# Kernel optimization log

Measured on AMD Instinct MI355X. Metric: run time of the kernel, lower is better.

## Reference

```python
import jax, jax.numpy as jnp
import numpy as np

S = 8      # max segment id present in masks
D = 768    # hidden size (hardcoded in the torch module)
N_VIS = 100  # leading vision tokens in vision_trace_feat


def _segment_mean(feat, mask, n_seg):
    """Per-(batch, seg_id) mean of feat tokens where mask == seg_id.
    feat: [B, L, D], mask: [B, L] ints in 0..n_seg. Returns means [B, n_seg, D], counts [B, n_seg].
    Equivalent to the torch loop over seg_id + split + per-chunk mean(dim=0)."""
    onehot = (mask[:, :, None] == jnp.arange(1, n_seg + 1)[None, None, :]).astype(feat.dtype)  # [B,L,S]
    sums = jnp.einsum('bls,bld->bsd', onehot, feat)   # [B,S,D]
    counts = onehot.sum(axis=1)                        # [B,S]
    means = sums / jnp.maximum(counts, 1.0)[:, :, None]
    return means, counts


def setup_inputs() -> dict:
    key = jax.random.key(0)
    k1, k2, k3, k4, k5, k6 = jax.random.split(key, 6)
    B = 64
    vision_trace_feat = jax.random.normal(k1, (B, N_VIS + 412, D), dtype=jnp.float32)
    vision_trace_mask = jnp.sort(jax.random.randint(k2, (B, 412), 0, S + 1), axis=-1).astype(jnp.int32)
    caption_feat = jax.random.normal(k3, (B, 512, D), dtype=jnp.float32)
    caption_mask = jnp.sort(jax.random.randint(k4, (B, 513), 0, S + 1), axis=-1).astype(jnp.int32)
    vt_merge_w = jax.random.normal(k5, (2 * D, D), dtype=jnp.float32) * 0.02
    vt_merge_b = jax.random.normal(k6, (D,), dtype=jnp.float32) * 0.02
    return {
        'vision_trace_feat': vision_trace_feat,
        'vision_trace_mask': vision_trace_mask,
        'caption_feat': caption_feat,
        'caption_mask': caption_mask,
        'vt_merge_w': vt_merge_w,
        'vt_merge_b': vt_merge_b,
    }


def reference(vision_trace_feat, vision_trace_mask, caption_feat, caption_mask, vt_merge_w, vt_merge_b):
    # --- CaptionAggregator (meanpool) ---
    cm = caption_mask[:, 1:]                                   # drop CLS position
    c_means, c_counts = _segment_mean(caption_feat, cm, S)      # [B,S,D], [B,S]
    c_present = (c_counts > 0).astype(c_means.dtype)
    caption_out = c_means * c_present[:, :, None]               # dense form: empty segments zeroed

    # --- VisionTraceAggregator (meanpool) ---
    vision_feat = vision_trace_feat[:, :N_VIS].mean(axis=1)     # [B,D]
    trace_feat = vision_trace_feat[:, N_VIS:]                   # [B,Lt,D]
    t_means, t_counts = _segment_mean(trace_feat, vision_trace_mask, S)
    t_present = (t_counts > 0).astype(t_means.dtype)
    vt = jnp.concatenate(
        [t_means, jnp.broadcast_to(vision_feat[:, None, :], t_means.shape)], axis=-1)  # [B,S,2D]
    vt_out = (vt @ vt_merge_w + vt_merge_b) * t_present[:, :, None]
    return (caption_out, vt_out)
```

## Files before the change

### kernel.cpp

```cpp
#include <hip/hip_runtime.h>
#include <hip/hip_bf16.h>

#define SEGS   8
#define DIM    768
#define NVIS   100
#define BATCH  64
#define LTOK   512
#define NCHK   8
#define TPC    64

#define OFF_PCAP  0
#define OFF_PTRC  (OFF_PCAP + BATCH*NCHK*SEGS*DIM)
#define OFF_PVIS  (OFF_PTRC + BATCH*NCHK*SEGS*DIM)
#define OFF_PCCNT (OFF_PVIS + BATCH*2*DIM)
#define OFF_PTCNT (OFF_PCCNT + BATCH*NCHK*SEGS)
#define OFF_TMEAN (OFF_PTCNT + BATCH*NCHK*SEGS)
#define OFF_TCNT  (OFF_TMEAN + BATCH*9*DIM)


__global__ __launch_bounds__(384) void reduce_kernel(
    const float* __restrict__ vt_feat,
    const int* __restrict__ vt_mask,
    const float* __restrict__ cap_feat,
    const int* __restrict__ cap_mask,
    float* __restrict__ ws)
{
    const int bid  = blockIdx.x;
    const int type = bid >> 9;
    const int b    = (bid >> 3) & 63;
    const int ck   = bid & 7;
    const int tid  = threadIdx.x;
    const int team = tid / 192;
    const int t    = tid % 192;
    const int c0   = t * 4;

    __shared__ __align__(16) int msk[TPC];
    __shared__ int scnt[SEGS + 1];
    __shared__ __align__(16) float4 red[SEGS][192];
    __shared__ __align__(16) float4 redv[192];

    if (tid < SEGS + 1) scnt[tid] = 0;
    if (tid < TPC) {
        const int l = ck * TPC + tid;
        int m;
        if (type == 0) m = cap_mask[b * 513 + 1 + l];
        else           m = (l >= NVIS) ? vt_mask[b * 412 + (l - NVIS)] : 0;
        msk[tid] = m;
    }
    __syncthreads();
    if (tid < TPC) { const int m = msk[tid]; if (m > 0) atomicAdd(&scnt[m], 1); }

    float acc[SEGS][4];
#pragma unroll
    for (int s = 0; s < SEGS; ++s) { acc[s][0]=0.f; acc[s][1]=0.f; acc[s][2]=0.f; acc[s][3]=0.f; }
    float vacc[4] = {0.f, 0.f, 0.f, 0.f};
    float tmp[4]  = {0.f, 0.f, 0.f, 0.f};
    int cur = 0;

    const float* __restrict__ feat = (type == 0) ? cap_feat : vt_feat;
    const int tok0 = ck * TPC + team * 32;
    const size_t base = (size_t)b * LTOK * DIM + (size_t)c0;

    for (int j = 0; j < 32; j += 4) {
        const float* p = feat + base + (size_t)(tok0 + j) * DIM;
        float4 v[4];
#pragma unroll
        for (int u = 0; u < 4; ++u)
            v[u] = *reinterpret_cast<const float4*>(p + (size_t)u * DIM);
        const int4 m4 = *reinterpret_cast<const int4*>(&msk[team * 32 + j]);
        const int mm[4] = {m4.x, m4.y, m4.z, m4.w};
#pragma unroll
        for (int u = 0; u < 4; ++u) {
            const int l = tok0 + j + u;
            if (type == 1 && l < NVIS) {
                vacc[0] += v[u].x; vacc[1] += v[u].y; vacc[2] += v[u].z; vacc[3] += v[u].w;
            } else {
                const int m = __builtin_amdgcn_readfirstlane(mm[u]);
                if (m != cur) {
#pragma unroll
                    for (int s = 0; s < SEGS; ++s)
                        if (cur == s + 1) {
                            acc[s][0] += tmp[0]; acc[s][1] += tmp[1];
                            acc[s][2] += tmp[2]; acc[s][3] += tmp[3];
                        }
                    tmp[0] = 0.f; tmp[1] = 0.f; tmp[2] = 0.f; tmp[3] = 0.f;
                    cur = m;
                }
                tmp[0] += v[u].x; tmp[1] += v[u].y; tmp[2] += v[u].z; tmp[3] += v[u].w;
            }
        }
    }
#pragma unroll
    for (int s = 0; s < SEGS; ++s)
        if (cur == s + 1) {
            acc[s][0] += tmp[0]; acc[s][1] += tmp[1];
            acc[s][2] += tmp[2]; acc[s][3] += tmp[3];
        }

    if (team == 1) {
#pragma unroll
        for (int s = 0; s < SEGS; ++s)
            red[s][t] = make_float4(acc[s][0], acc[s][1], acc[s][2], acc[s][3]);
        redv[t] = make_float4(vacc[0], vacc[1], vacc[2], vacc[3]);
    }
    __syncthreads();

    if (team == 0) {
        float* __restrict__ pbase = ws + (type == 0 ? OFF_PCAP : OFF_PTRC)
                                  + ((size_t)(b * NCHK + ck) * SEGS) * DIM + c0;
#pragma unroll
        for (int s = 0; s < SEGS; ++s) {
            const float4 r1 = red[s][t];
            *reinterpret_cast<float4*>(pbase + s * DIM) =
                make_float4(acc[s][0] + r1.x, acc[s][1] + r1.y,
                            acc[s][2] + r1.z, acc[s][3] + r1.w);
        }
        if (t < SEGS) {
            int* __restrict__ cbase = (int*)(ws + (type == 0 ? OFF_PCCNT : OFF_PTCNT))
                                    + (b * NCHK + ck) * SEGS;
            cbase[t] = scnt[t + 1];
        }
        if (type == 1 && ck < 2) {
            const float4 r1 = redv[t];
            *reinterpret_cast<float4*>(ws + OFF_PVIS + (size_t)(b * 2 + ck) * DIM + c0) =
                make_float4(vacc[0] + r1.x, vacc[1] + r1.y,
                            vacc[2] + r1.z, vacc[3] + r1.w);
        }
    }
}

__global__ __launch_bounds__(256) void combine1_kernel(
    const float* __restrict__ ws_c, float* __restrict__ ws,
    float* __restrict__ out)
{
    const int i = blockIdx.x * 256 + threadIdx.x;
    const int N1 = BATCH * SEGS * DIM / 4;
    if (i < N1) {
        const int b  = i / 1536;
        const int r  = i % 1536;
        const int s  = r / 192;
        const int d4 = (r % 192) * 4;
        float4 sum = make_float4(0.f, 0.f, 0.f, 0.f); int c = 0;
#pragma unroll
        for (int ck = 0; ck < NCHK; ++ck) {
            const float4 v = *reinterpret_cast<const float4*>(
                ws_c + OFF_PCAP + ((size_t)((b * NCHK + ck) * SEGS + s)) * DIM + d4);
            sum.x += v.x; sum.y += v.y; sum.z += v.z; sum.w += v.w;
            c += ((const int*)(ws_c + OFF_PCCNT))[(b * NCHK + ck) * SEGS + s];
        }
        float4 o = make_float4(0.f, 0.f, 0.f, 0.f);
        if (c > 0) {
            const float fc = (float)c;
            o = make_float4(sum.x / fc, sum.y / fc, sum.z / fc, sum.w / fc);
        }
        reinterpret_cast<float4*>(out)[i] = o;
    } else if (i < 2 * N1) {
        const int j  = i - N1;
        const int b  = j / 1536;
        const int r  = j % 1536;
        const int s  = r / 192;
        const int d4 = (r % 192) * 4;
        float4 sum = make_float4(0.f, 0.f, 0.f, 0.f); int c = 0;
#pragma unroll
        for (int ck = 0; ck < NCHK; ++ck) {
            const float4 v = *reinterpret_cast<const float4*>(
                ws_c + OFF_PTRC + ((size_t)((b * NCHK + ck) * SEGS + s)) * DIM + d4);
            sum.x += v.x; sum.y += v.y; sum.z += v.z; sum.w += v.w;
            c += ((const int*)(ws_c + OFF_PTCNT))[(b * NCHK + ck) * SEGS + s];
        }
        float4 m = make_float4(0.f, 0.f, 0.f, 0.f);
        if (c > 0) {
            const float fc = (float)c;
            m = make_float4(sum.x / fc, sum.y / fc, sum.z / fc, sum.w / fc);
        }
        *reinterpret_cast<float4*>(ws + OFF_TMEAN + ((size_t)(b * 9 + s)) * DIM + d4) = m;
        if (d4 == 0) ((int*)(ws + OFF_TCNT))[b * SEGS + s] = c;
    } else {
        const int j  = i - 2 * N1;
        const int b  = j / 192;
        const int d4 = (j % 192) * 4;
        const float4 v0 = *reinterpret_cast<const float4*>(
            ws_c + OFF_PVIS + (size_t)(b * 2 + 0) * DIM + d4);
        const float4 v1 = *reinterpret_cast<const float4*>(
            ws_c + OFF_PVIS + (size_t)(b * 2 + 1) * DIM + d4);
        const float sc = 1.0f / (float)NVIS;
        *reinterpret_cast<float4*>(ws + OFF_TMEAN + ((size_t)(b * 9 + 8)) * DIM + d4) =
            make_float4((v0.x + v1.x) * sc, (v0.y + v1.y) * sc,
                        (v0.z + v1.z) * sc, (v0.w + v1.w) * sc);
    }
}

__global__ __launch_bounds__(192) void gemm2_kernel(
    const float* __restrict__ W,
    const float* __restrict__ bias,
    const float* __restrict__ ws_c,
    float* __restrict__ out)
{
    const int b   = blockIdx.x >> 3;
    const int nc  = blockIdx.x & 7;
    const int n0  = nc * 96;
    const int tid = threadIdx.x;
    const int cg  = tid % 24;
    const int kq  = tid / 24;
    const int d0  = n0 + cg * 4;

    __shared__ __align__(16) float tm[9 * 8 * 100];
    __shared__ __align__(16) float red[192 * 9 * 4];

    for (int idx = tid; idx < 9 * DIM / 4; idx += 192) {
        const int r   = idx / 192;
        const int rem = idx % 192;
        const int kq_ = rem / 24;
        const int kk4 = rem % 24;
        const float4 v = reinterpret_cast<const float4*>(
            ws_c + OFF_TMEAN + (size_t)b * 9 * DIM)[idx];
        *reinterpret_cast<float4*>(&tm[(r * 8 + kq_) * 100 + kk4 * 4]) = v;
    }
    __syncthreads();

    float acc[9][4];
#pragma unroll
    for (int r = 0; r < 9; ++r) { acc[r][0]=0.f; acc[r][1]=0.f; acc[r][2]=0.f; acc[r][3]=0.f; }

    const float* __restrict__ Wt = W + (size_t)(kq * 96) * DIM + d0;
    const float* __restrict__ Wb = W + (size_t)(DIM + kq * 96) * DIM + d0;

    for (int kk = 0; kk < 96; kk += 4) {
        float4 wt[4], wb[4];
#pragma unroll
        for (int u = 0; u < 4; ++u) {
            wt[u] = *reinterpret_cast<const float4*>(Wt + (size_t)(kk + u) * DIM);
            wb[u] = *reinterpret_cast<const float4*>(Wb + (size_t)(kk + u) * DIM);
        }
        float a[9][4];
#pragma unroll
        for (int r = 0; r < 9; ++r) {
            const float4 t = *reinterpret_cast<const float4*>(&tm[(r * 8 + kq) * 100 + kk]);
            a[r][0] = t.x; a[r][1] = t.y; a[r][2] = t.z; a[r][3] = t.w;
        }
#pragma unroll
        for (int u = 0; u < 4; ++u) {
            const float t4[4] = {wt[u].x, wt[u].y, wt[u].z, wt[u].w};
            const float b4[4] = {wb[u].x, wb[u].y, wb[u].z, wb[u].w};
#pragma unroll
            for (int r = 0; r < SEGS; ++r) {
#pragma unroll
                for (int j = 0; j < 4; ++j) acc[r][j] += a[r][u] * t4[j];
            }
#pragma unroll
            for (int j = 0; j < 4; ++j) acc[8][j] += a[8][u] * b4[j];
        }
    }

#pragma unroll
    for (int r = 0; r < 9; ++r)
        *reinterpret_cast<float4*>(&red[(tid * 9 + r) * 4]) =
            make_float4(acc[r][0], acc[r][1], acc[r][2], acc[r][3]);
    __syncthreads();

    {
        const int cg2 = tid >> 3;
        const int s   = tid & 7;
        float4 sumS = make_float4(0.f, 0.f, 0.f, 0.f);
        float4 sumV = make_float4(0.f, 0.f, 0.f, 0.f);
#pragma unroll
        for (int q = 0; q < 8; ++q) {
            const int base = (q * 24 + cg2) * 9;
            const float4 vS = *reinterpret_cast<const float4*>(&red[(base + s) * 4]);
            const float4 vV = *reinterpret_cast<const float4*>(&red[(base + 8) * 4]);
            sumS.x += vS.x; sumS.y += vS.y; sumS.z += vS.z; sumS.w += vS.w;
            sumV.x += vV.x; sumV.y += vV.y; sumV.z += vV.z; sumV.w += vV.w;
        }
        const int dd = n0 + cg2 * 4;
        const int c  = ((const int*)(ws_c + OFF_TCNT))[b * SEGS + s];
        float4 o = make_float4(0.f, 0.f, 0.f, 0.f);
        if (c > 0) {
            const float4 bb = *reinterpret_cast<const float4*>(bias + dd);
            o = make_float4(sumS.x + sumV.x + bb.x, sumS.y + sumV.y + bb.y,
                            sumS.z + sumV.z + bb.z, sumS.w + sumV.w + bb.w);
        }
        *reinterpret_cast<float4*>(out + (size_t)BATCH * SEGS * DIM
                                   + ((size_t)(b * SEGS + s)) * DIM + dd) = o;
    }
}

extern "C" void kernel_launch(void* const* d_in, const int* in_sizes, int n_in,
                              void* d_out, int out_size, void* d_ws, size_t ws_size,
                              hipStream_t stream) {
    const float* vt_feat  = (const float*)d_in[0];
    const int*   vt_mask  = (const int*)d_in[1];
    const float* cap_feat = (const float*)d_in[2];
    const int*   cap_mask = (const int*)d_in[3];
    const float* W        = (const float*)d_in[4];
    const float* bias     = (const float*)d_in[5];
    float* out = (float*)d_out;
    float* ws = (float*)d_ws;

    reduce_kernel  <<<1024, 384, 0, stream>>>(vt_feat, vt_mask, cap_feat, cap_mask, ws);
    combine1_kernel<<<816, 256, 0, stream>>>(ws, ws, out);
    gemm2_kernel   <<<512, 192, 0, stream>>>(W, bias, ws, out);
}
```

Baseline: 260.6 us.

## Fuse segment reduction and combine into one kernel splitting by column blocks

Replaces the token-chunked reduce kernel plus combine kernel with a single kernel where each block owns a batch and a 256-column slice over all 512 tokens. Eight wavefront teams reduce through shared memory and write the final means directly, which removes the partial-sum workspace round trip and one kernel launch. Each team also skips its leading run of zero-mask tokens, since those contribute to no segment. The cost is fewer blocks (384 instead of 1024) and more shared memory per block, which may lower the parallelism available for streaming the feature data.

New measurement: 251.4 us. 1.04x faster.

```diff
diff --git a/kernel.cpp b/kernel.cpp
--- a/kernel.cpp
+++ b/kernel.cpp
@@ -6,49 +6,57 @@
 #define NVIS   100
 #define BATCH  64
 #define LTOK   512
-#define NCHK   8
-#define TPC    64
-
-#define OFF_PCAP  0
-#define OFF_PTRC  (OFF_PCAP + BATCH*NCHK*SEGS*DIM)
-#define OFF_PVIS  (OFF_PTRC + BATCH*NCHK*SEGS*DIM)
-#define OFF_PCCNT (OFF_PVIS + BATCH*2*DIM)
-#define OFF_PTCNT (OFF_PCCNT + BATCH*NCHK*SEGS)
-#define OFF_TMEAN (OFF_PTCNT + BATCH*NCHK*SEGS)
+
+#define OFF_TMEAN 0
 #define OFF_TCNT  (OFF_TMEAN + BATCH*9*DIM)
 
 
-__global__ __launch_bounds__(384) void reduce_kernel(
+__global__ __launch_bounds__(512) void reduce_merge_kernel(
     const float* __restrict__ vt_feat,
     const int* __restrict__ vt_mask,
     const float* __restrict__ cap_feat,
     const int* __restrict__ cap_mask,
-    float* __restrict__ ws)
+    float* __restrict__ ws,
+    float* __restrict__ out)
 {
     const int bid  = blockIdx.x;
-    const int type = bid >> 9;
-    const int b    = (bid >> 3) & 63;
-    const int ck   = bid & 7;
+    const int type = bid / 192;
+    const int rr   = bid % 192;
+    const int b    = rr / 3;
+    const int cb   = rr % 3;
     const int tid  = threadIdx.x;
-    const int team = tid / 192;
-    const int t    = tid % 192;
-    const int c0   = t * 4;
-
-    __shared__ __align__(16) int msk[TPC];
+    const int team = tid >> 6;
+    const int t    = tid & 63;
+    const int c0   = cb * 256 + t * 4;
+
+    __shared__ __align__(16) int msk[LTOK];
     __shared__ int scnt[SEGS + 1];
-    __shared__ __align__(16) float4 red[SEGS][192];
-    __shared__ __align__(16) float4 redv[192];
+    __shared__ __align__(16) float4 red[7][SEGS][64];
+    __shared__ __align__(16) float4 redv[7][64];
 
     if (tid < SEGS + 1) scnt[tid] = 0;
-    if (tid < TPC) {
-        const int l = ck * TPC + tid;
-        int m;
-        if (type == 0) m = cap_mask[b * 513 + 1 + l];
-        else           m = (l >= NVIS) ? vt_mask[b * 412 + (l - NVIS)] : 0;
-        msk[tid] = m;
-    }
-    __syncthreads();
-    if (tid < TPC) { const int m = msk[tid]; if (m > 0) atomicAdd(&scnt[m], 1); }
+    int m0;
+    {
+        const int l = tid;
+        if (type == 0) m0 = cap_mask[b * 513 + 1 + l];
+        else           m0 = (l >= NVIS) ? vt_mask[b * 412 + (l - NVIS)] : 0;
+        msk[l] = m0;
+    }
+    __syncthreads();
+    if (m0 > 0) atomicAdd(&scnt[m0], 1);
+
+    const int tok0 = team * 64;
+    int j0 = 0;
+    if (type == 0) {
+        while (j0 < 64 && msk[tok0 + j0] == 0) ++j0;
+    } else {
+        while (j0 < 64) {
+            const int l = tok0 + j0;
+            if (l < NVIS || msk[l] > 0) break;
+            ++j0;
+        }
+    }
+    j0 &= ~3;
 
     float acc[SEGS][4];
 #pragma unroll
@@ -58,16 +66,15 @@
     int cur = 0;
 
     const float* __restrict__ feat = (type == 0) ? cap_feat : vt_feat;
-    const int tok0 = ck * TPC + team * 32;
     const size_t base = (size_t)b * LTOK * DIM + (size_t)c0;
 
-    for (int j = 0; j < 32; j += 4) {
+    for (int j = j0; j < 64; j += 4) {
         const float* p = feat + base + (size_t)(tok0 + j) * DIM;
         float4 v[4];
 #pragma unroll
         for (int u = 0; u < 4; ++u)
             v[u] = *reinterpret_cast<const float4*>(p + (size_t)u * DIM);
-        const int4 m4 = *reinterpret_cast<const int4*>(&msk[team * 32 + j]);
+        const int4 m4 = *reinterpret_cast<const int4*>(&msk[tok0 + j]);
         const int mm[4] = {m4.x, m4.y, m4.z, m4.w};
 #pragma unroll
         for (int u = 0; u < 4; ++u) {
@@ -97,96 +104,60 @@
             acc[s][2] += tmp[2]; acc[s][3] += tmp[3];
         }
 
-    if (team == 1) {
+    if (team > 0) {
 #pragma unroll
         for (int s = 0; s < SEGS; ++s)
-            red[s][t] = make_float4(acc[s][0], acc[s][1], acc[s][2], acc[s][3]);
-        redv[t] = make_float4(vacc[0], vacc[1], vacc[2], vacc[3]);
+            red[team - 1][s][t] = make_float4(acc[s][0], acc[s][1], acc[s][2], acc[s][3]);
+        redv[team - 1][t] = make_float4(vacc[0], vacc[1], vacc[2], vacc[3]);
     }
     __syncthreads();
 
     if (team == 0) {
-        float* __restrict__ pbase = ws + (type == 0 ? OFF_PCAP : OFF_PTRC)
-                                  + ((size_t)(b * NCHK + ck) * SEGS) * DIM + c0;
 #pragma unroll
         for (int s = 0; s < SEGS; ++s) {
-            const float4 r1 = red[s][t];
-            *reinterpret_cast<float4*>(pbase + s * DIM) =
-                make_float4(acc[s][0] + r1.x, acc[s][1] + r1.y,
-                            acc[s][2] + r1.z, acc[s][3] + r1.w);
-        }
-        if (t < SEGS) {
-            int* __restrict__ cbase = (int*)(ws + (type == 0 ? OFF_PCCNT : OFF_PTCNT))
-                                    + (b * NCHK + ck) * SEGS;
-            cbase[t] = scnt[t + 1];
-        }
-        if (type == 1 && ck < 2) {
-            const float4 r1 = redv[t];
-            *reinterpret_cast<float4*>(ws + OFF_PVIS + (size_t)(b * 2 + ck) * DIM + c0) =
-                make_float4(vacc[0] + r1.x, vacc[1] + r1.y,
-                            vacc[2] + r1.z, vacc[3] + r1.w);
-        }
-    }
-}
-
-__global__ __launch_bounds__(256) void combine1_kernel(
-    const float* __restrict__ ws_c, float* __restrict__ ws,
-    float* __restrict__ out)
-{
-    const int i = blockIdx.x * 256 + threadIdx.x;
-    const int N1 = BATCH * SEGS * DIM / 4;
-    if (i < N1) {
-        const int b  = i / 1536;
-        const int r  = i % 1536;
-        const int s  = r / 192;
-        const int d4 = (r % 192) * 4;
-        float4 sum = make_float4(0.f, 0.f, 0.f, 0.f); int c = 0;
-#pragma unroll
-        for (int ck = 0; ck < NCHK; ++ck) {
-            const float4 v = *reinterpret_cast<const float4*>(
-                ws_c + OFF_PCAP + ((size_t)((b * NCHK + ck) * SEGS + s)) * DIM + d4);
-            sum.x += v.x; sum.y += v.y; sum.z += v.z; sum.w += v.w;
-            c += ((const int*)(ws_c + OFF_PCCNT))[(b * NCHK + ck) * SEGS + s];
-        }
-        float4 o = make_float4(0.f, 0.f, 0.f, 0.f);
-        if (c > 0) {
-            const float fc = (float)c;
-            o = make_float4(sum.x / fc, sum.y / fc, sum.z / fc, sum.w / fc);
-        }
-        reinterpret_cast<float4*>(out)[i] = o;
-    } else if (i < 2 * N1) {
-        const int j  = i - N1;
-        const int b  = j / 1536;
-        const int r  = j % 1536;
-        const int s  = r / 192;
-        const int d4 = (r % 192) * 4;
-        float4 sum = make_float4(0.f, 0.f, 0.f, 0.f); int c = 0;
-#pragma unroll
-        for (int ck = 0; ck < NCHK; ++ck) {
-            const float4 v = *reinterpret_cast<const float4*>(
-                ws_c + OFF_PTRC + ((size_t)((b * NCHK + ck) * SEGS + s)) * DIM + d4);
-            sum.x += v.x; sum.y += v.y; sum.z += v.z; sum.w += v.w;
-            c += ((const int*)(ws_c + OFF_PTCNT))[(b * NCHK + ck) * SEGS + s];
-        }
-        float4 m = make_float4(0.f, 0.f, 0.f, 0.f);
-        if (c > 0) {
-            const float fc = (float)c;
-            m = make_float4(sum.x / fc, sum.y / fc, sum.z / fc, sum.w / fc);
-        }
-        *reinterpret_cast<float4*>(ws + OFF_TMEAN + ((size_t)(b * 9 + s)) * DIM + d4) = m;
-        if (d4 == 0) ((int*)(ws + OFF_TCNT))[b * SEGS + s] = c;
-    } else {
-        const int j  = i - 2 * N1;
-        const int b  = j / 192;
-        const int d4 = (j % 192) * 4;
-        const float4 v0 = *reinterpret_cast<const float4*>(
-            ws_c + OFF_PVIS + (size_t)(b * 2 + 0) * DIM + d4);
-        const float4 v1 = *reinterpret_cast<const float4*>(
-            ws_c + OFF_PVIS + (size_t)(b * 2 + 1) * DIM + d4);
-        const float sc = 1.0f / (float)NVIS;
-        *reinterpret_cast<float4*>(ws + OFF_TMEAN + ((size_t)(b * 9 + 8)) * DIM + d4) =
-            make_float4((v0.x + v1.x) * sc, (v0.y + v1.y) * sc,
-                        (v0.z + v1.z) * sc, (v0.w + v1.w) * sc);
+#pragma unroll
+            for (int q = 0; q < 7; ++q) {
+                const float4 r1 = red[q][s][t];
+                acc[s][0] += r1.x; acc[s][1] += r1.y; acc[s][2] += r1.z; acc[s][3] += r1.w;
+            }
+        }
+        if (type == 0) {
+            float* __restrict__ o = out + ((size_t)b * SEGS) * DIM + c0;
+#pragma unroll
+            for (int s = 0; s < SEGS; ++s) {
+                const int c = scnt[s + 1];
+                float4 w = make_float4(0.f, 0.f, 0.f, 0.f);
+                if (c > 0) {
+                    const float ic = 1.0f / (float)c;
+                    w = make_float4(acc[s][0] * ic, acc[s][1] * ic,
+                                    acc[s][2] * ic, acc[s][3] * ic);
+                }
+                *reinterpret_cast<float4*>(o + s * DIM) = w;
+            }
+        } else {
+#pragma unroll
+            for (int q = 0; q < 7; ++q) {
+                const float4 r1 = redv[q][t];
+                vacc[0] += r1.x; vacc[1] += r1.y; vacc[2] += r1.z; vacc[3] += r1.w;
+            }
+            float* __restrict__ tm = ws + OFF_TMEAN + (size_t)b * 9 * DIM + c0;
+#pragma unroll
+            for (int s = 0; s < SEGS; ++s) {
+                const int c = scnt[s + 1];
+                float4 w = make_float4(0.f, 0.f, 0.f, 0.f);
+                if (c > 0) {
+                    const float ic = 1.0f / (float)c;
+                    w = make_float4(acc[s][0] * ic, acc[s][1] * ic,
+                                    acc[s][2] * ic, acc[s][3] * ic);
+                }
+                *reinterpret_cast<float4*>(tm + s * DIM) = w;
+            }
+            const float sc = 1.0f / (float)NVIS;
+            *reinterpret_cast<float4*>(tm + 8 * DIM) =
+                make_float4(vacc[0] * sc, vacc[1] * sc, vacc[2] * sc, vacc[3] * sc);
+            if (cb == 0 && t < SEGS)
+                ((int*)(ws + OFF_TCNT))[b * SEGS + t] = scnt[t + 1];
+        }
     }
 }
 
@@ -296,7 +267,6 @@
     float* out = (float*)d_out;
     float* ws = (float*)d_ws;
 
-    reduce_kernel  <<<1024, 384, 0, stream>>>(vt_feat, vt_mask, cap_feat, cap_mask, ws);
-    combine1_kernel<<<816, 256, 0, stream>>>(ws, ws, out);
-    gemm2_kernel   <<<512, 192, 0, stream>>>(W, bias, ws, out);
+    reduce_merge_kernel<<<384, 512, 0, stream>>>(vt_feat, vt_mask, cap_feat, cap_mask, ws, out);
+    gemm2_kernel       <<<512, 192, 0, stream>>>(W, bias, ws, out);
 }
```
